# Kernel tuning notes

Measured on AMD Instinct MI355X. Metric: run time of the kernel, lower is better.

## Reference

```python
import jax, jax.numpy as jnp
import numpy as np

B, T, I, H, L = 32, 1024, 1024, 1024, 3


def setup_inputs() -> dict:
    key = jax.random.key(0)
    ks = jax.random.split(key, 8)
    sc_in = 1.0 / np.sqrt(I)
    sc_h = 1.0 / np.sqrt(H)
    return {
        "x": jax.random.normal(ks[0], (B, T, I), dtype=jnp.float32),
        "s0": jnp.zeros((B, H), dtype=jnp.float32),
        "w_h": jax.random.normal(ks[1], (I, H), dtype=jnp.float32) * sc_in,
        "w_t": jax.random.normal(ks[2], (I, H), dtype=jnp.float32) * sc_in,
        "w_c": jax.random.normal(ks[3], (I, H), dtype=jnp.float32) * sc_in,
        "Rh": jax.random.normal(ks[4], (L, H, H), dtype=jnp.float32) * sc_h,
        "Rt": jax.random.normal(ks[5], (L, H, H), dtype=jnp.float32) * sc_h,
        "Rc": jax.random.normal(ks[6], (L, H, H), dtype=jnp.float32) * sc_h,
        "bh": jnp.zeros((L, H), dtype=jnp.float32),
        "bt": jnp.zeros((L, H), dtype=jnp.float32),
        "bc": jnp.zeros((L, H), dtype=jnp.float32),
    }


def reference(x, s0, w_h, w_t, w_c, Rh, Rt, Rc, bh, bt, bc):
    # x: [B, T, I]; s0: [B, H]. Dropout prob = 0 -> identity.
    num_layers = Rh.shape[0]

    def step(s, x_t):
        # Input projections only feed layer 0 (as in the torch code).
        whx = x_t @ w_h  # [B, H]
        wtx = x_t @ w_t
        wcx = x_t @ w_c
        for l in range(num_layers):
            h_in = (whx if l == 0 else 0.0) + s @ Rh[l].T + bh[l]
            t_in = (wtx if l == 0 else 0.0) + s @ Rt[l].T + bt[l]
            c_in = (wcx if l == 0 else 0.0) + s @ Rc[l].T + bc[l]
            h = jnp.tanh(h_in)
            t = jax.nn.sigmoid(t_in)
            c = jax.nn.sigmoid(c_in)
            s = h * t + s * c
        return s, s

    x_tbi = jnp.swapaxes(x, 0, 1)  # [T, B, I] for scan over time
    s_T, outs = jax.lax.scan(step, s0, x_tbi)
    return jnp.swapaxes(outs, 0, 1), s_T  # ([B, T, H], [B, H])
```

## Files before the change

kernel.cpp:

```cpp
#include <hip/hip_runtime.h>
#include <hip/hip_bf16.h>

static constexpr int Bb = 32;
static constexpr int Tt = 1024;
static constexpr int Ii = 1024;
static constexpr int Hh = 1024;
static constexpr int NWG = 256;

static constexpr int SLOT_E = Hh * Bb;
static constexpr int NSLOT  = 3 * Tt + 1;

typedef float f4 __attribute__((ext_vector_type(4)));

static constexpr int LDS_WORDS = 36 * 1024 + 4 * 12 * 32;
static constexpr int LDS_BYTES = LDS_WORDS * 4;

template <typename PT> __device__ __forceinline__ float pt_to_f(PT v);
template <> __device__ __forceinline__ float pt_to_f<float>(float v) { return v; }
template <> __device__ __forceinline__ float pt_to_f<__hip_bfloat16>(__hip_bfloat16 v) { return __bfloat162float(v); }

template <typename PT> __device__ __forceinline__ PT f_to_pt(float v);
template <> __device__ __forceinline__ float f_to_pt<float>(float v) { return v; }
template <> __device__ __forceinline__ __hip_bfloat16 f_to_pt<__hip_bfloat16>(float v) { return __float2bfloat16(v); }

#define CGLD(dst, p, lit) \
    asm volatile("global_load_dwordx4 %0, %1, off offset:" lit : "=v"(dst) : "v"(p))
#define GB(sv, p, a,b,c,d2,e,f,g2,h) \
    CGLD(sv[0],p,a); CGLD(sv[1],p,b); CGLD(sv[2],p,c); CGLD(sv[3],p,d2); \
    CGLD(sv[4],p,e); CGLD(sv[5],p,f); CGLD(sv[6],p,g2); CGLD(sv[7],p,h)
#define VWAIT(n) do { asm volatile("s_waitcnt vmcnt(" #n ")" ::: "memory"); \
                      __builtin_amdgcn_sched_barrier(0); } while (0)

template <typename PT>
__global__ __launch_bounds__(256, 2) void proj_gemm(
    const float* __restrict__ X, const float* __restrict__ Wh,
    const float* __restrict__ Wt, const float* __restrict__ Wc,
    PT* __restrict__ P2)
{
    __shared__ float smem[4160];
    float* As = smem;
    float* Bs = smem + 1088;

    const int tid = threadIdx.x;
    const int tx = tid & 15, ty = tid >> 4;
    const int col0 = blockIdx.x * 64;
    const int t0 = blockIdx.y * 2;

    float acc[3][4][4];
#pragma unroll
    for (int g = 0; g < 3; ++g)
#pragma unroll
        for (int mm = 0; mm < 4; ++mm)
#pragma unroll
            for (int nn = 0; nn < 4; ++nn) acc[g][mm][nn] = 0.f;

    const int lm = tid >> 2, lk4 = (tid & 3) * 4;
    const float* aptr = X + ((size_t)(lm & 31) * Tt + (t0 + (lm >> 5))) * Ii + lk4;
    const int bk = tid >> 4, bn4 = (tid & 15) * 4;

    for (int k0 = 0; k0 < Ii; k0 += 16) {
        float4 av = *(const float4*)(aptr + k0);
        As[(lk4 + 0) * 68 + lm] = av.x;
        As[(lk4 + 1) * 68 + lm] = av.y;
        As[(lk4 + 2) * 68 + lm] = av.z;
        As[(lk4 + 3) * 68 + lm] = av.w;
        *(float4*)&Bs[0 * 1024 + bk * 64 + bn4] = *(const float4*)(Wh + (size_t)(k0 + bk) * Hh + col0 + bn4);
        *(float4*)&Bs[1 * 1024 + bk * 64 + bn4] = *(const float4*)(Wt + (size_t)(k0 + bk) * Hh + col0 + bn4);
        *(float4*)&Bs[2 * 1024 + bk * 64 + bn4] = *(const float4*)(Wc + (size_t)(k0 + bk) * Hh + col0 + bn4);
        __syncthreads();
#pragma unroll
        for (int k = 0; k < 16; ++k) {
            float4 a = *(const float4*)&As[k * 68 + ty * 4];
            float a_[4] = {a.x, a.y, a.z, a.w};
#pragma unroll
            for (int g = 0; g < 3; ++g) {
                float4 b = *(const float4*)&Bs[g * 1024 + k * 64 + tx * 4];
                float b_[4] = {b.x, b.y, b.z, b.w};
#pragma unroll
                for (int mm = 0; mm < 4; ++mm)
#pragma unroll
                    for (int nn = 0; nn < 4; ++nn)
                        acc[g][mm][nn] += a_[mm] * b_[nn];
            }
        }
        __syncthreads();
    }

    float* E = smem;
    const int b4 = (tid & 7) * 4;
#pragma unroll 1
    for (int g = 0; g < 3; ++g) {
        __syncthreads();
#pragma unroll
        for (int mm = 0; mm < 4; ++mm)
#pragma unroll
            for (int nn = 0; nn < 4; ++nn)
                E[(ty * 4 + mm) * 65 + tx * 4 + nn] = acc[g][mm][nn];
        __syncthreads();
        PT* dst = P2 + (size_t)g * Tt * Hh * Bb;
#pragma unroll
        for (int it = 0; it < 4; ++it) {
            const int line = (tid >> 3) + it * 32;
            const int tt = line >> 6, hh = line & 63;
            const float o0 = E[(tt * 32 + b4 + 0) * 65 + hh];
            const float o1 = E[(tt * 32 + b4 + 1) * 65 + hh];
            const float o2v = E[(tt * 32 + b4 + 2) * 65 + hh];
            const float o3 = E[(tt * 32 + b4 + 3) * 65 + hh];
            PT* d = dst + ((size_t)(t0 + tt) * Hh + col0 + hh) * Bb + b4;
            d[0] = f_to_pt<PT>(o0); d[1] = f_to_pt<PT>(o1);
            d[2] = f_to_pt<PT>(o2v); d[3] = f_to_pt<PT>(o3);
        }
    }
}

template <typename RT>
__global__ void init_k(const float* __restrict__ s0, RT* __restrict__ ring0,
                       unsigned* __restrict__ flags)
{
    const int i = blockIdx.x * 256 + threadIdx.x;
    if (i < Bb * Hh) { const int b = i >> 10, h = i & 1023; ring0[h * 32 + b] = f_to_pt<RT>(s0[i]); }
    if (i < 256) flags[i] = 0;
}

template <typename RT>
__global__ __launch_bounds__(256) void out_transpose(
    const RT* __restrict__ ring, float* __restrict__ out, float* __restrict__ sT)
{
    __shared__ float tile[128 * 33];
    const int tid = threadIdx.x;
    const int h0 = blockIdx.x * 128;
    const int t = blockIdx.y;
    const RT* src = ring + (size_t)(3 * t + 3) * SLOT_E + h0 * 32;
#pragma unroll
    for (int e = 0; e < 16; ++e) {
        const int idx = e * 256 + tid;
        tile[(idx >> 5) * 33 + (idx & 31)] = pt_to_f<RT>(src[idx]);
    }
    __syncthreads();
    const int hi = tid & 31, bq = tid >> 5;
#pragma unroll
    for (int e = 0; e < 4; ++e) {
        const int b = bq + e * 8;
        float4 v;
        v.x = tile[(hi * 4 + 0) * 33 + b];
        v.y = tile[(hi * 4 + 1) * 33 + b];
        v.z = tile[(hi * 4 + 2) * 33 + b];
        v.w = tile[(hi * 4 + 3) * 33 + b];
        *(float4*)(out + ((size_t)b * Tt + t) * Hh + h0 + hi * 4) = v;
        if (t == Tt - 1) *(float4*)(sT + (size_t)b * Hh + h0 + hi * 4) = v;
    }
}

template <typename PT, typename RT>
__global__ __launch_bounds__(256, 1) void rhn_recur(
    const float* __restrict__ Rh, const float* __restrict__ Rt,
    const float* __restrict__ Rc, const float* __restrict__ bh,
    const float* __restrict__ bt, const float* __restrict__ bc,
    const PT* __restrict__ P2, RT* __restrict__ ring,
    unsigned* __restrict__ flags)
{
    extern __shared__ float lds[];
    float* part = lds + 36 * 1024;

    const int g = blockIdx.x;
    const int tid = threadIdx.x;

    {
        const int k4 = tid * 4;
        const int sk = k4 ^ (((k4 >> 5) & 7) << 2);
#pragma unroll 1
        for (int j = 0; j < 36; ++j) {
            const int l = j / 12;
            const int rem = j - l * 12;
            const int gt = rem >> 2;
            const int q = rem & 3;
            const int h = (q << 8) | g;
            const float* src = (gt == 0 ? Rh : (gt == 1 ? Rt : Rc)) + ((size_t)l * Hh + h) * Hh;
            *(float4*)&lds[(j << 10) | sk] = *(const float4*)(src + k4);
        }
    }
    __syncthreads();

    const int ks = tid >> 3;
    const int b0 = (tid & 7) << 2;
    const int q8 = ks & 7;
    const int wv = tid >> 6;
    const int ub = tid & 31;
    const int uqc = (tid >> 5) & 3;
    const int uhc = (uqc << 8) | g;

    int o2[8];
#pragma unroll
    for (int c = 0; c < 8; ++c) o2[c] = ((c ^ q8) << 2);

    float brh[3], brt[3], brc[3];
#pragma unroll
    for (int l = 0; l < 3; ++l) {
        brh[l] = bh[l * Hh + uhc];
        brt[l] = bt[l * Hh + uhc];
        brc[l] = bc[l * Hh + uhc];
    }

    float so_reg = pt_to_f<RT>(ring[uhc * 32 + ub]);

#pragma unroll 1
    for (int t = 0; t < Tt; ++t) {
#pragma unroll 1
        for (int l = 0; l < 3; ++l) {
            const int p = t * 3 + l;

            float pv0 = 0.f, pv1 = 0.f, pv2 = 0.f;
            if (l == 0 && tid < 128) {
                const size_t pb = ((size_t)t * Hh + uhc) * Bb + ub;
                pv0 = pt_to_f<PT>(P2[pb]);
                pv1 = pt_to_f<PT>(P2[(size_t)Tt * Hh * Bb + pb]);
                pv2 = pt_to_f<PT>(P2[2 * (size_t)Tt * Hh * Bb + pb]);
            }

            const float* rp = lds + l * 12288 + (ks << 5);

            f4 accv[12];
#pragma unroll
            for (int jj = 0; jj < 12; ++jj) accv[jj] = (f4){0.f, 0.f, 0.f, 0.f};

            if constexpr (sizeof(RT) == 4) {
                const float* sA = (const float*)ring + (size_t)p * SLOT_E + (ks << 5) * 32 + b0;
                f4 sv0[8], sv1[8];
                GB(sv0, sA, "0","128","256","384","512","640","768","896");
                GB(sv1, sA, "1024","1152","1280","1408","1536","1664","1792","1920");
                VWAIT(8);
#pragma unroll
                for (int jj = 0; jj < 12; ++jj) {
                    const f4 r0 = *(const f4*)(rp + jj * 1024 + o2[0]);
                    const f4 r1 = *(const f4*)(rp + jj * 1024 + o2[1]);
                    f4 a = accv[jj];
                    a += sv0[0] * r0[0]; a += sv0[1] * r0[1]; a += sv0[2] * r0[2]; a += sv0[3] * r0[3];
                    a += sv0[4] * r1[0]; a += sv0[5] * r1[1]; a += sv0[6] * r1[2]; a += sv0[7] * r1[3];
                    accv[jj] = a;
                }
                GB(sv0, sA, "2048","2176","2304","2432","2560","2688","2816","2944");
                VWAIT(8);
#pragma unroll
                for (int jj = 0; jj < 12; ++jj) {
                    const f4 r0 = *(const f4*)(rp + jj * 1024 + o2[2]);
                    const f4 r1 = *(const f4*)(rp + jj * 1024 + o2[3]);
                    f4 a = accv[jj];
                    a += sv1[0] * r0[0]; a += sv1[1] * r0[1]; a += sv1[2] * r0[2]; a += sv1[3] * r0[3];
                    a += sv1[4] * r1[0]; a += sv1[5] * r1[1]; a += sv1[6] * r1[2]; a += sv1[7] * r1[3];
                    accv[jj] = a;
                }
                GB(sv1, sA, "3072","3200","3328","3456","3584","3712","3840","3968");
                VWAIT(8);
#pragma unroll
                for (int jj = 0; jj < 12; ++jj) {
                    const f4 r0 = *(const f4*)(rp + jj * 1024 + o2[4]);
                    const f4 r1 = *(const f4*)(rp + jj * 1024 + o2[5]);
                    f4 a = accv[jj];
                    a += sv0[0] * r0[0]; a += sv0[1] * r0[1]; a += sv0[2] * r0[2]; a += sv0[3] * r0[3];
                    a += sv0[4] * r1[0]; a += sv0[5] * r1[1]; a += sv0[6] * r1[2]; a += sv0[7] * r1[3];
                    accv[jj] = a;
                }
                VWAIT(0);
#pragma unroll
                for (int jj = 0; jj < 12; ++jj) {
                    const f4 r0 = *(const f4*)(rp + jj * 1024 + o2[6]);
                    const f4 r1 = *(const f4*)(rp + jj * 1024 + o2[7]);
                    f4 a = accv[jj];
                    a += sv1[0] * r0[0]; a += sv1[1] * r0[1]; a += sv1[2] * r0[2]; a += sv1[3] * r0[3];
                    a += sv1[4] * r1[0]; a += sv1[5] * r1[1]; a += sv1[6] * r1[2]; a += sv1[7] * r1[3];
                    accv[jj] = a;
                }
            } else {
                const __hip_bfloat16* sIn = (const __hip_bfloat16*)ring + (size_t)p * SLOT_E + (ks << 5) * 32 + b0;
#pragma unroll
                for (int blk = 0; blk < 4; ++blk) {
                    f4 sv[8];
#pragma unroll
                    for (int i = 0; i < 8; ++i) {
                        const ushort4 u = *(const ushort4*)(sIn + (blk * 8 + i) * 32);
                        sv[i][0] = __uint_as_float((unsigned)u.x << 16);
                        sv[i][1] = __uint_as_float((unsigned)u.y << 16);
                        sv[i][2] = __uint_as_float((unsigned)u.z << 16);
                        sv[i][3] = __uint_as_float((unsigned)u.w << 16);
                    }
#pragma unroll
                    for (int jj = 0; jj < 12; ++jj) {
                        const f4 r0 = *(const f4*)(rp + jj * 1024 + o2[blk * 2]);
                        const f4 r1 = *(const f4*)(rp + jj * 1024 + o2[blk * 2 + 1]);
                        f4 a = accv[jj];
                        a += sv[0] * r0[0]; a += sv[1] * r0[1]; a += sv[2] * r0[2]; a += sv[3] * r0[3];
                        a += sv[4] * r1[0]; a += sv[5] * r1[1]; a += sv[6] * r1[2]; a += sv[7] * r1[3];
                        accv[jj] = a;
                    }
                }
            }

#pragma unroll
            for (int jj = 0; jj < 12; ++jj) {
#pragma unroll
                for (int st = 8; st <= 32; st <<= 1) {
                    accv[jj][0] += __shfl_xor(accv[jj][0], st);
                    accv[jj][1] += __shfl_xor(accv[jj][1], st);
                    accv[jj][2] += __shfl_xor(accv[jj][2], st);
                    accv[jj][3] += __shfl_xor(accv[jj][3], st);
                }
            }
            f4 s1 = accv[0];
#pragma unroll
            for (int j2 = 1; j2 < 8; ++j2) if (q8 == j2) s1 = accv[j2];
            f4 s2 = accv[8];
#pragma unroll
            for (int j2 = 1; j2 < 4; ++j2) if (q8 == j2) s2 = accv[8 + j2];
            *(f4*)&part[(wv * 12 + q8) * 32 + b0] = s1;
            if (q8 < 4) *(f4*)&part[(wv * 12 + 8 + q8) * 32 + b0] = s2;
            __syncthreads();

            if (tid < 128) {
                float vals[3];
#pragma unroll
                for (int gt = 0; gt < 3; ++gt) {
                    const int jl = (gt << 2) + uqc;
                    vals[gt] = part[jl * 32 + ub] + part[(12 + jl) * 32 + ub]
                             + part[(24 + jl) * 32 + ub] + part[(36 + jl) * 32 + ub];
                }
                float bb0, bb1, bb2;
                if (l == 0)      { bb0 = brh[0]; bb1 = brt[0]; bb2 = brc[0]; }
                else if (l == 1) { bb0 = brh[1]; bb1 = brt[1]; bb2 = brc[1]; }
                else             { bb0 = brh[2]; bb1 = brt[2]; bb2 = brc[2]; }
                vals[0] += bb0; vals[1] += bb1; vals[2] += bb2;
                if (l == 0) { vals[0] += pv0; vals[1] += pv1; vals[2] += pv2; }
                const float hv = 1.f - 2.f / (1.f + __expf(2.f * vals[0]));
                const float tv = 1.f / (1.f + __expf(-vals[1]));
                const float cv = 1.f / (1.f + __expf(-vals[2]));
                const float sn = hv * tv + so_reg * cv;
                so_reg = sn;
                RT* wp = ring + (size_t)(p + 1) * SLOT_E + uhc * 32 + ub;
                if constexpr (sizeof(RT) == 4) {
                    __hip_atomic_store((float*)wp, sn, __ATOMIC_RELAXED, __HIP_MEMORY_SCOPE_AGENT);
                } else {
                    __hip_bfloat16 b16 = __float2bfloat16(sn);
                    __hip_atomic_store((unsigned short*)wp, *(unsigned short*)&b16,
                                       __ATOMIC_RELAXED, __HIP_MEMORY_SCOPE_AGENT);
                }
            }

            const unsigned ph = (unsigned)(p + 1);
            __syncthreads();
            if (tid == 0)
                __hip_atomic_store(&flags[g], ph, __ATOMIC_RELAXED, __HIP_MEMORY_SCOPE_AGENT);
            if (tid < 64) {
                for (;;) {
                    const unsigned v0 = __hip_atomic_load(&flags[tid],       __ATOMIC_RELAXED, __HIP_MEMORY_SCOPE_AGENT);
                    const unsigned v1 = __hip_atomic_load(&flags[tid + 64],  __ATOMIC_RELAXED, __HIP_MEMORY_SCOPE_AGENT);
                    const unsigned v2 = __hip_atomic_load(&flags[tid + 128], __ATOMIC_RELAXED, __HIP_MEMORY_SCOPE_AGENT);
                    const unsigned v3 = __hip_atomic_load(&flags[tid + 192], __ATOMIC_RELAXED, __HIP_MEMORY_SCOPE_AGENT);
                    if (__all((int)((v0 >= ph) & (v1 >= ph) & (v2 >= ph) & (v3 >= ph)))) break;
                    __builtin_amdgcn_s_sleep(2);
                }
            }
            __syncthreads();
        }
    }
}

extern "C" void kernel_launch(void* const* d_in, const int* in_sizes, int n_in,
                              void* d_out, int out_size, void* d_ws, size_t ws_size,
                              hipStream_t stream)
{
    (void)in_sizes; (void)n_in; (void)out_size;
    const float* x  = (const float*)d_in[0];
    const float* s0 = (const float*)d_in[1];
    const float* wh = (const float*)d_in[2];
    const float* wt = (const float*)d_in[3];
    const float* wc = (const float*)d_in[4];
    const float* Rh = (const float*)d_in[5];
    const float* Rt = (const float*)d_in[6];
    const float* Rc = (const float*)d_in[7];
    const float* bh = (const float*)d_in[8];
    const float* bt = (const float*)d_in[9];
    const float* bc = (const float*)d_in[10];

    float* out = (float*)d_out;
    float* sT  = out + (size_t)Bb * Tt * Hh;

    const size_t THB  = (size_t)Tt * Hh * Bb;
    const size_t p2f  = 3 * THB * 4, p2h = 3 * THB * 2;
    const size_t ringF = (size_t)NSLOT * SLOT_E * 4;
    const size_t ringH = (size_t)NSLOT * SLOT_E * 2;
    const size_t tail = 4096;

    char* w = (char*)d_ws;

    if (ws_size >= p2f + ringF + tail) {
        float* P2 = (float*)w;
        float* ring = (float*)(w + p2f);
        unsigned* flags = (unsigned*)(w + p2f + ringF);
        proj_gemm<float><<<dim3(16, 512), 256, 0, stream>>>(x, wh, wt, wc, P2);
        init_k<float><<<128, 256, 0, stream>>>(s0, ring, flags);
        hipFuncSetAttribute(reinterpret_cast<const void*>(rhn_recur<float, float>),
                            hipFuncAttributeMaxDynamicSharedMemorySize, LDS_BYTES);
        void* args[] = {(void*)&Rh, (void*)&Rt, (void*)&Rc, (void*)&bh, (void*)&bt, (void*)&bc,
                        (void*)&P2, (void*)&ring, (void*)&flags};
        hipLaunchCooperativeKernel(reinterpret_cast<void*>(rhn_recur<float, float>),
                                   dim3(NWG), dim3(256), args, LDS_BYTES, stream);
        out_transpose<float><<<dim3(8, 1024), 256, 0, stream>>>(ring, out, sT);
    } else if (ws_size >= p2h + ringF + tail) {
        __hip_bfloat16* P2 = (__hip_bfloat16*)w;
        float* ring = (float*)(w + p2h);
        unsigned* flags = (unsigned*)(w + p2h + ringF);
        proj_gemm<__hip_bfloat16><<<dim3(16, 512), 256, 0, stream>>>(x, wh, wt, wc, P2);
        init_k<float><<<128, 256, 0, stream>>>(s0, ring, flags);
        hipFuncSetAttribute(reinterpret_cast<const void*>(rhn_recur<__hip_bfloat16, float>),
                            hipFuncAttributeMaxDynamicSharedMemorySize, LDS_BYTES);
        void* args[] = {(void*)&Rh, (void*)&Rt, (void*)&Rc, (void*)&bh, (void*)&bt, (void*)&bc,
                        (void*)&P2, (void*)&ring, (void*)&flags};
        hipLaunchCooperativeKernel(reinterpret_cast<void*>(rhn_recur<__hip_bfloat16, float>),
                                   dim3(NWG), dim3(256), args, LDS_BYTES, stream);
        out_transpose<float><<<dim3(8, 1024), 256, 0, stream>>>(ring, out, sT);
    } else {
        __hip_bfloat16* P2 = (__hip_bfloat16*)w;
        __hip_bfloat16* ring = (__hip_bfloat16*)(w + p2h);
        unsigned* flags = (unsigned*)(w + p2h + ringH);
        proj_gemm<__hip_bfloat16><<<dim3(16, 512), 256, 0, stream>>>(x, wh, wt, wc, P2);
        init_k<__hip_bfloat16><<<128, 256, 0, stream>>>(s0, ring, flags);
        hipFuncSetAttribute(reinterpret_cast<const void*>(rhn_recur<__hip_bfloat16, __hip_bfloat16>),
                            hipFuncAttributeMaxDynamicSharedMemorySize, LDS_BYTES);
        void* args[] = {(void*)&Rh, (void*)&Rt, (void*)&Rc, (void*)&bh, (void*)&bt, (void*)&bc,
                        (void*)&P2, (void*)&ring, (void*)&flags};
        hipLaunchCooperativeKernel(reinterpret_cast<void*>(rhn_recur<__hip_bfloat16, __hip_bfloat16>),
                                   dim3(NWG), dim3(256), args, LDS_BYTES, stream);
        out_transpose<__hip_bfloat16><<<dim3(8, 1024), 256, 0, stream>>>(ring, out, sT);
    }
}
```

Measured before the change: 33.73 ms.

## Split batch into two independent halves with separate grid barriers to overlap sync

The recurrent kernel now splits the 32-sequence batch into two 16-sequence halves, each with its own state ring layout and its own set of per-workgroup flags. Each workgroup alternates between the halves, so the grid-wide barrier for one half can settle while the other half is computing. The aim is to hide the latency of the global flag barrier, which sits on the critical path of every one of the 3*T layer steps. In exchange there are twice as many barriers and smaller per-step work, and the flags are now cleared with a memset instead of inside the init kernel.

Result: no change. 33.34 ms (-1.2%).

```diff
diff --git a/kernel.cpp b/kernel.cpp
--- a/kernel.cpp
+++ b/kernel.cpp
@@ -7,13 +7,15 @@
 static constexpr int Hh = 1024;
 static constexpr int NWG = 256;
 
-static constexpr int SLOT_E = Hh * Bb;
-static constexpr int NSLOT  = 3 * Tt + 1;
+static constexpr int HSLOT = Hh * 16;
+static constexpr int NSLOT2 = 2 * (3 * Tt + 1);
 
 typedef float f4 __attribute__((ext_vector_type(4)));
 
-static constexpr int LDS_WORDS = 36 * 1024 + 4 * 12 * 32;
+static constexpr int LDS_WORDS = 36 * 1024 + 4 * 12 * 16;
 static constexpr int LDS_BYTES = LDS_WORDS * 4;
+
+static constexpr int SYNC_BYTES = 4096;
 
 template <typename PT> __device__ __forceinline__ float pt_to_f(PT v);
 template <> __device__ __forceinline__ float pt_to_f<float>(float v) { return v; }
@@ -25,9 +27,8 @@
 
 #define CGLD(dst, p, lit) \
     asm volatile("global_load_dwordx4 %0, %1, off offset:" lit : "=v"(dst) : "v"(p))
-#define GB(sv, p, a,b,c,d2,e,f,g2,h) \
-    CGLD(sv[0],p,a); CGLD(sv[1],p,b); CGLD(sv[2],p,c); CGLD(sv[3],p,d2); \
-    CGLD(sv[4],p,e); CGLD(sv[5],p,f); CGLD(sv[6],p,g2); CGLD(sv[7],p,h)
+#define GB4(sv, p, a,b,c,d2) \
+    CGLD(sv[0],p,a); CGLD(sv[1],p,b); CGLD(sv[2],p,c); CGLD(sv[3],p,d2)
 #define VWAIT(n) do { asm volatile("s_waitcnt vmcnt(" #n ")" ::: "memory"); \
                       __builtin_amdgcn_sched_barrier(0); } while (0)
 
@@ -114,12 +115,14 @@
 }
 
 template <typename RT>
-__global__ void init_k(const float* __restrict__ s0, RT* __restrict__ ring0,
-                       unsigned* __restrict__ flags)
+__global__ void init_k(const float* __restrict__ s0, RT* __restrict__ ring)
 {
     const int i = blockIdx.x * 256 + threadIdx.x;
-    if (i < Bb * Hh) { const int b = i >> 10, h = i & 1023; ring0[h * 32 + b] = f_to_pt<RT>(s0[i]); }
-    if (i < 256) flags[i] = 0;
+    if (i < Bb * Hh) {
+        const int b = i >> 10, h = i & 1023;
+        const int grp = b >> 4, bl = b & 15;
+        ring[(size_t)grp * HSLOT + h * 16 + bl] = f_to_pt<RT>(s0[i]);
+    }
 }
 
 template <typename RT>
@@ -130,11 +133,15 @@
     const int tid = threadIdx.x;
     const int h0 = blockIdx.x * 128;
     const int t = blockIdx.y;
-    const RT* src = ring + (size_t)(3 * t + 3) * SLOT_E + h0 * 32;
+    const RT* srcA = ring + (size_t)((3 * t + 3) * 2) * HSLOT + h0 * 16;
+    const RT* srcB = srcA + HSLOT;
 #pragma unroll
     for (int e = 0; e < 16; ++e) {
         const int idx = e * 256 + tid;
-        tile[(idx >> 5) * 33 + (idx & 31)] = pt_to_f<RT>(src[idx]);
+        const int h = idx >> 5, b = idx & 31;
+        const float v = (b < 16) ? pt_to_f<RT>(srcA[h * 16 + b])
+                                 : pt_to_f<RT>(srcB[h * 16 + (b - 16)]);
+        tile[h * 33 + b] = v;
     }
     __syncthreads();
     const int hi = tid & 31, bq = tid >> 5;
@@ -151,13 +158,28 @@
     }
 }
 
+__device__ __forceinline__ void poll256(unsigned* flags, int tid, unsigned ph)
+{
+    if (tid < 64) {
+        for (;;) {
+            const unsigned v0 = __hip_atomic_load(&flags[tid],       __ATOMIC_RELAXED, __HIP_MEMORY_SCOPE_AGENT);
+            const unsigned v1 = __hip_atomic_load(&flags[tid + 64],  __ATOMIC_RELAXED, __HIP_MEMORY_SCOPE_AGENT);
+            const unsigned v2 = __hip_atomic_load(&flags[tid + 128], __ATOMIC_RELAXED, __HIP_MEMORY_SCOPE_AGENT);
+            const unsigned v3 = __hip_atomic_load(&flags[tid + 192], __ATOMIC_RELAXED, __HIP_MEMORY_SCOPE_AGENT);
+            if (__all((int)((v0 >= ph) & (v1 >= ph) & (v2 >= ph) & (v3 >= ph)))) break;
+            __builtin_amdgcn_s_sleep(2);
+        }
+    }
+    __syncthreads();
+}
+
 template <typename PT, typename RT>
 __global__ __launch_bounds__(256, 1) void rhn_recur(
     const float* __restrict__ Rh, const float* __restrict__ Rt,
     const float* __restrict__ Rc, const float* __restrict__ bh,
     const float* __restrict__ bt, const float* __restrict__ bc,
     const PT* __restrict__ P2, RT* __restrict__ ring,
-    unsigned* __restrict__ flags)
+    unsigned* __restrict__ flagsA, unsigned* __restrict__ flagsB)
 {
     extern __shared__ float lds[];
     float* part = lds + 36 * 1024;
@@ -167,7 +189,7 @@
 
     {
         const int k4 = tid * 4;
-        const int sk = k4 ^ (((k4 >> 5) & 7) << 2);
+        const int sk = k4 ^ (((k4 >> 5) & 3) << 2);
 #pragma unroll 1
         for (int j = 0; j < 36; ++j) {
             const int l = j / 12;
@@ -181,17 +203,19 @@
     }
     __syncthreads();
 
-    const int ks = tid >> 3;
-    const int b0 = (tid & 7) << 2;
-    const int q8 = ks & 7;
+    const int ks = tid >> 2;
+    const int bq = tid & 3;
+    const int b0 = bq << 2;
     const int wv = tid >> 6;
-    const int ub = tid & 31;
-    const int uqc = (tid >> 5) & 3;
-    const int uhc = (uqc << 8) | g;
-
-    int o2[8];
-#pragma unroll
-    for (int c = 0; c < 8; ++c) o2[c] = ((c ^ q8) << 2);
+    const int jsel = ks & 15;
+    const int ubb = tid & 15;
+    const int uq  = (tid >> 4) & 3;
+    const int uhc = (uq << 8) | g;
+
+    int o2[4];
+#pragma unroll
+    for (int c = 0; c < 4; ++c)
+        o2[c] = (((ks << 4) | (c << 2))) ^ ((((ks << 4) >> 5) & 3) << 2);
 
     float brh[3], brt[3], brc[3];
 #pragma unroll
@@ -201,164 +225,162 @@
         brc[l] = bc[l * Hh + uhc];
     }
 
-    float so_reg = pt_to_f<RT>(ring[uhc * 32 + ub]);
+    float soA = pt_to_f<RT>(ring[uhc * 16 + ubb]);
+    float soB = pt_to_f<RT>(ring[(size_t)HSLOT + uhc * 16 + ubb]);
+
+    const size_t THB = (size_t)Tt * Hh * Bb;
+    float pvA0 = 0.f, pvA1 = 0.f, pvA2 = 0.f, pvB0 = 0.f, pvB1 = 0.f, pvB2 = 0.f;
+    auto loadP = [&](int tt) {
+        if (tid < 64) {
+            const size_t pb = ((size_t)tt * Hh + uhc) * Bb + ubb;
+            pvA0 = pt_to_f<PT>(P2[pb]);
+            pvA1 = pt_to_f<PT>(P2[THB + pb]);
+            pvA2 = pt_to_f<PT>(P2[2 * THB + pb]);
+            pvB0 = pt_to_f<PT>(P2[pb + 16]);
+            pvB1 = pt_to_f<PT>(P2[THB + pb + 16]);
+            pvB2 = pt_to_f<PT>(P2[2 * THB + pb + 16]);
+        }
+    };
+    loadP(0);
+
+    auto halfstep = [&](const float* rp, const RT* rs, RT* rw, float& so,
+                        float pv0, float pv1, float pv2, bool addP,
+                        float bb0, float bb1, float bb2) {
+        f4 accv[12];
+#pragma unroll
+        for (int jj = 0; jj < 12; ++jj) accv[jj] = (f4){0.f, 0.f, 0.f, 0.f};
+
+        if constexpr (sizeof(RT) == 4) {
+            const float* sA = (const float*)rs + (size_t)(ks << 4) * 16 + b0;
+            f4 sv0[4], sv1[4], sv2[4], sv3[4];
+            GB4(sv0, sA, "0","64","128","192");
+            GB4(sv1, sA, "256","320","384","448");
+            GB4(sv2, sA, "512","576","640","704");
+            GB4(sv3, sA, "768","832","896","960");
+            VWAIT(12);
+#pragma unroll
+            for (int jj = 0; jj < 12; ++jj) {
+                const f4 r = *(const f4*)(rp + jj * 1024 + o2[0]);
+                f4 a = accv[jj];
+                a += sv0[0] * r[0]; a += sv0[1] * r[1]; a += sv0[2] * r[2]; a += sv0[3] * r[3];
+                accv[jj] = a;
+            }
+            VWAIT(8);
+#pragma unroll
+            for (int jj = 0; jj < 12; ++jj) {
+                const f4 r = *(const f4*)(rp + jj * 1024 + o2[1]);
+                f4 a = accv[jj];
+                a += sv1[0] * r[0]; a += sv1[1] * r[1]; a += sv1[2] * r[2]; a += sv1[3] * r[3];
+                accv[jj] = a;
+            }
+            VWAIT(4);
+#pragma unroll
+            for (int jj = 0; jj < 12; ++jj) {
+                const f4 r = *(const f4*)(rp + jj * 1024 + o2[2]);
+                f4 a = accv[jj];
+                a += sv2[0] * r[0]; a += sv2[1] * r[1]; a += sv2[2] * r[2]; a += sv2[3] * r[3];
+                accv[jj] = a;
+            }
+            VWAIT(0);
+#pragma unroll
+            for (int jj = 0; jj < 12; ++jj) {
+                const f4 r = *(const f4*)(rp + jj * 1024 + o2[3]);
+                f4 a = accv[jj];
+                a += sv3[0] * r[0]; a += sv3[1] * r[1]; a += sv3[2] * r[2]; a += sv3[3] * r[3];
+                accv[jj] = a;
+            }
+        } else {
+            const __hip_bfloat16* sIn = (const __hip_bfloat16*)rs + (size_t)(ks << 4) * 16 + b0;
+#pragma unroll
+            for (int blk = 0; blk < 4; ++blk) {
+                f4 sv[4];
+#pragma unroll
+                for (int i = 0; i < 4; ++i) {
+                    const ushort4 u = *(const ushort4*)(sIn + (size_t)(blk * 4 + i) * 16);
+                    sv[i][0] = __uint_as_float((unsigned)u.x << 16);
+                    sv[i][1] = __uint_as_float((unsigned)u.y << 16);
+                    sv[i][2] = __uint_as_float((unsigned)u.z << 16);
+                    sv[i][3] = __uint_as_float((unsigned)u.w << 16);
+                }
+#pragma unroll
+                for (int jj = 0; jj < 12; ++jj) {
+                    const f4 r = *(const f4*)(rp + jj * 1024 + o2[blk]);
+                    f4 a = accv[jj];
+                    a += sv[0] * r[0]; a += sv[1] * r[1]; a += sv[2] * r[2]; a += sv[3] * r[3];
+                    accv[jj] = a;
+                }
+            }
+        }
+
+#pragma unroll
+        for (int jj = 0; jj < 12; ++jj) {
+#pragma unroll
+            for (int st = 4; st <= 32; st <<= 1) {
+                accv[jj][0] += __shfl_xor(accv[jj][0], st);
+                accv[jj][1] += __shfl_xor(accv[jj][1], st);
+                accv[jj][2] += __shfl_xor(accv[jj][2], st);
+                accv[jj][3] += __shfl_xor(accv[jj][3], st);
+            }
+        }
+        f4 s1 = accv[0];
+#pragma unroll
+        for (int j2 = 1; j2 < 12; ++j2) if (jsel == j2) s1 = accv[j2];
+        if (jsel < 12) *(f4*)&part[wv * 192 + jsel * 16 + b0] = s1;
+        __syncthreads();
+
+        if (tid < 64) {
+            float vals[3];
+#pragma unroll
+            for (int gt = 0; gt < 3; ++gt) {
+                const int jl = (gt << 2) + uq;
+                vals[gt] = part[jl * 16 + ubb] + part[192 + jl * 16 + ubb]
+                         + part[384 + jl * 16 + ubb] + part[576 + jl * 16 + ubb];
+            }
+            vals[0] += bb0; vals[1] += bb1; vals[2] += bb2;
+            if (addP) { vals[0] += pv0; vals[1] += pv1; vals[2] += pv2; }
+            const float hv = 1.f - 2.f / (1.f + __expf(2.f * vals[0]));
+            const float tv = 1.f / (1.f + __expf(-vals[1]));
+            const float cv = 1.f / (1.f + __expf(-vals[2]));
+            const float sn = hv * tv + so * cv;
+            so = sn;
+            RT* wp = rw + uhc * 16 + ubb;
+            if constexpr (sizeof(RT) == 4) {
+                __hip_atomic_store((float*)wp, sn, __ATOMIC_RELAXED, __HIP_MEMORY_SCOPE_AGENT);
+            } else {
+                __hip_bfloat16 b16 = __float2bfloat16(sn);
+                __hip_atomic_store((unsigned short*)wp, *(unsigned short*)&b16,
+                                   __ATOMIC_RELAXED, __HIP_MEMORY_SCOPE_AGENT);
+            }
+        }
+        __syncthreads();
+    };
 
 #pragma unroll 1
     for (int t = 0; t < Tt; ++t) {
 #pragma unroll 1
         for (int l = 0; l < 3; ++l) {
             const int p = t * 3 + l;
-
-            float pv0 = 0.f, pv1 = 0.f, pv2 = 0.f;
-            if (l == 0 && tid < 128) {
-                const size_t pb = ((size_t)t * Hh + uhc) * Bb + ub;
-                pv0 = pt_to_f<PT>(P2[pb]);
-                pv1 = pt_to_f<PT>(P2[(size_t)Tt * Hh * Bb + pb]);
-                pv2 = pt_to_f<PT>(P2[2 * (size_t)Tt * Hh * Bb + pb]);
-            }
-
-            const float* rp = lds + l * 12288 + (ks << 5);
-
-            f4 accv[12];
-#pragma unroll
-            for (int jj = 0; jj < 12; ++jj) accv[jj] = (f4){0.f, 0.f, 0.f, 0.f};
-
-            if constexpr (sizeof(RT) == 4) {
-                const float* sA = (const float*)ring + (size_t)p * SLOT_E + (ks << 5) * 32 + b0;
-                f4 sv0[8], sv1[8];
-                GB(sv0, sA, "0","128","256","384","512","640","768","896");
-                GB(sv1, sA, "1024","1152","1280","1408","1536","1664","1792","1920");
-                VWAIT(8);
-#pragma unroll
-                for (int jj = 0; jj < 12; ++jj) {
-                    const f4 r0 = *(const f4*)(rp + jj * 1024 + o2[0]);
-                    const f4 r1 = *(const f4*)(rp + jj * 1024 + o2[1]);
-                    f4 a = accv[jj];
-                    a += sv0[0] * r0[0]; a += sv0[1] * r0[1]; a += sv0[2] * r0[2]; a += sv0[3] * r0[3];
-                    a += sv0[4] * r1[0]; a += sv0[5] * r1[1]; a += sv0[6] * r1[2]; a += sv0[7] * r1[3];
-                    accv[jj] = a;
-                }
-                GB(sv0, sA, "2048","2176","2304","2432","2560","2688","2816","2944");
-                VWAIT(8);
-#pragma unroll
-                for (int jj = 0; jj < 12; ++jj) {
-                    const f4 r0 = *(const f4*)(rp + jj * 1024 + o2[2]);
-                    const f4 r1 = *(const f4*)(rp + jj * 1024 + o2[3]);
-                    f4 a = accv[jj];
-                    a += sv1[0] * r0[0]; a += sv1[1] * r0[1]; a += sv1[2] * r0[2]; a += sv1[3] * r0[3];
-                    a += sv1[4] * r1[0]; a += sv1[5] * r1[1]; a += sv1[6] * r1[2]; a += sv1[7] * r1[3];
-                    accv[jj] = a;
-                }
-                GB(sv1, sA, "3072","3200","3328","3456","3584","3712","3840","3968");
-                VWAIT(8);
-#pragma unroll
-                for (int jj = 0; jj < 12; ++jj) {
-                    const f4 r0 = *(const f4*)(rp + jj * 1024 + o2[4]);
-                    const f4 r1 = *(const f4*)(rp + jj * 1024 + o2[5]);
-                    f4 a = accv[jj];
-                    a += sv0[0] * r0[0]; a += sv0[1] * r0[1]; a += sv0[2] * r0[2]; a += sv0[3] * r0[3];
-                    a += sv0[4] * r1[0]; a += sv0[5] * r1[1]; a += sv0[6] * r1[2]; a += sv0[7] * r1[3];
-                    accv[jj] = a;
-                }
-                VWAIT(0);
-#pragma unroll
-                for (int jj = 0; jj < 12; ++jj) {
-                    const f4 r0 = *(const f4*)(rp + jj * 1024 + o2[6]);
-                    const f4 r1 = *(const f4*)(rp + jj * 1024 + o2[7]);
-                    f4 a = accv[jj];
-                    a += sv1[0] * r0[0]; a += sv1[1] * r0[1]; a += sv1[2] * r0[2]; a += sv1[3] * r0[3];
-                    a += sv1[4] * r1[0]; a += sv1[5] * r1[1]; a += sv1[6] * r1[2]; a += sv1[7] * r1[3];
-                    accv[jj] = a;
-                }
-            } else {
-                const __hip_bfloat16* sIn = (const __hip_bfloat16*)ring + (size_t)p * SLOT_E + (ks << 5) * 32 + b0;
-#pragma unroll
-                for (int blk = 0; blk < 4; ++blk) {
-                    f4 sv[8];
-#pragma unroll
-                    for (int i = 0; i < 8; ++i) {
-                        const ushort4 u = *(const ushort4*)(sIn + (blk * 8 + i) * 32);
-                        sv[i][0] = __uint_as_float((unsigned)u.x << 16);
-                        sv[i][1] = __uint_as_float((unsigned)u.y << 16);
-                        sv[i][2] = __uint_as_float((unsigned)u.z << 16);
-                        sv[i][3] = __uint_as_float((unsigned)u.w << 16);
-                    }
-#pragma unroll
-                    for (int jj = 0; jj < 12; ++jj) {
-                        const f4 r0 = *(const f4*)(rp + jj * 1024 + o2[blk * 2]);
-                        const f4 r1 = *(const f4*)(rp + jj * 1024 + o2[blk * 2 + 1]);
-                        f4 a = accv[jj];
-                        a += sv[0] * r0[0]; a += sv[1] * r0[1]; a += sv[2] * r0[2]; a += sv[3] * r0[3];
-                        a += sv[4] * r1[0]; a += sv[5] * r1[1]; a += sv[6] * r1[2]; a += sv[7] * r1[3];
-                        accv[jj] = a;
-                    }
-                }
-            }
-
-#pragma unroll
-            for (int jj = 0; jj < 12; ++jj) {
-#pragma unroll
-                for (int st = 8; st <= 32; st <<= 1) {
-                    accv[jj][0] += __shfl_xor(accv[jj][0], st);
-                    accv[jj][1] += __shfl_xor(accv[jj][1], st);
-                    accv[jj][2] += __shfl_xor(accv[jj][2], st);
-                    accv[jj][3] += __shfl_xor(accv[jj][3], st);
-                }
-            }
-            f4 s1 = accv[0];
-#pragma unroll
-            for (int j2 = 1; j2 < 8; ++j2) if (q8 == j2) s1 = accv[j2];
-            f4 s2 = accv[8];
-#pragma unroll
-            for (int j2 = 1; j2 < 4; ++j2) if (q8 == j2) s2 = accv[8 + j2];
-            *(f4*)&part[(wv * 12 + q8) * 32 + b0] = s1;
-            if (q8 < 4) *(f4*)&part[(wv * 12 + 8 + q8) * 32 + b0] = s2;
-            __syncthreads();
-
-            if (tid < 128) {
-                float vals[3];
-#pragma unroll
-                for (int gt = 0; gt < 3; ++gt) {
-                    const int jl = (gt << 2) + uqc;
-                    vals[gt] = part[jl * 32 + ub] + part[(12 + jl) * 32 + ub]
-                             + part[(24 + jl) * 32 + ub] + part[(36 + jl) * 32 + ub];
-                }
-                float bb0, bb1, bb2;
-                if (l == 0)      { bb0 = brh[0]; bb1 = brt[0]; bb2 = brc[0]; }
-                else if (l == 1) { bb0 = brh[1]; bb1 = brt[1]; bb2 = brc[1]; }
-                else             { bb0 = brh[2]; bb1 = brt[2]; bb2 = brc[2]; }
-                vals[0] += bb0; vals[1] += bb1; vals[2] += bb2;
-                if (l == 0) { vals[0] += pv0; vals[1] += pv1; vals[2] += pv2; }
-                const float hv = 1.f - 2.f / (1.f + __expf(2.f * vals[0]));
-                const float tv = 1.f / (1.f + __expf(-vals[1]));
-                const float cv = 1.f / (1.f + __expf(-vals[2]));
-                const float sn = hv * tv + so_reg * cv;
-                so_reg = sn;
-                RT* wp = ring + (size_t)(p + 1) * SLOT_E + uhc * 32 + ub;
-                if constexpr (sizeof(RT) == 4) {
-                    __hip_atomic_store((float*)wp, sn, __ATOMIC_RELAXED, __HIP_MEMORY_SCOPE_AGENT);
-                } else {
-                    __hip_bfloat16 b16 = __float2bfloat16(sn);
-                    __hip_atomic_store((unsigned short*)wp, *(unsigned short*)&b16,
-                                       __ATOMIC_RELAXED, __HIP_MEMORY_SCOPE_AGENT);
-                }
-            }
-
-            const unsigned ph = (unsigned)(p + 1);
-            __syncthreads();
+            float bb0, bb1, bb2;
+            if (l == 0)      { bb0 = brh[0]; bb1 = brt[0]; bb2 = brc[0]; }
+            else if (l == 1) { bb0 = brh[1]; bb1 = brt[1]; bb2 = brc[1]; }
+            else             { bb0 = brh[2]; bb1 = brt[2]; bb2 = brc[2]; }
+            const float* rp = lds + l * 12288;
+
+            poll256(flagsA, tid, (unsigned)p);
+            halfstep(rp, ring + (size_t)(p * 2 + 0) * HSLOT,
+                         ring + (size_t)((p + 1) * 2 + 0) * HSLOT,
+                     soA, pvA0, pvA1, pvA2, l == 0, bb0, bb1, bb2);
             if (tid == 0)
-                __hip_atomic_store(&flags[g], ph, __ATOMIC_RELAXED, __HIP_MEMORY_SCOPE_AGENT);
-            if (tid < 64) {
-                for (;;) {
-                    const unsigned v0 = __hip_atomic_load(&flags[tid],       __ATOMIC_RELAXED, __HIP_MEMORY_SCOPE_AGENT);
-                    const unsigned v1 = __hip_atomic_load(&flags[tid + 64],  __ATOMIC_RELAXED, __HIP_MEMORY_SCOPE_AGENT);
-                    const unsigned v2 = __hip_atomic_load(&flags[tid + 128], __ATOMIC_RELAXED, __HIP_MEMORY_SCOPE_AGENT);
-                    const unsigned v3 = __hip_atomic_load(&flags[tid + 192], __ATOMIC_RELAXED, __HIP_MEMORY_SCOPE_AGENT);
-                    if (__all((int)((v0 >= ph) & (v1 >= ph) & (v2 >= ph) & (v3 >= ph)))) break;
-                    __builtin_amdgcn_s_sleep(2);
-                }
-            }
-            __syncthreads();
+                __hip_atomic_store(&flagsA[g], (unsigned)(p + 1), __ATOMIC_RELAXED, __HIP_MEMORY_SCOPE_AGENT);
+
+            poll256(flagsB, tid, (unsigned)p);
+            halfstep(rp, ring + (size_t)(p * 2 + 1) * HSLOT,
+                         ring + (size_t)((p + 1) * 2 + 1) * HSLOT,
+                     soB, pvB0, pvB1, pvB2, l == 0, bb0, bb1, bb2);
+            if (tid == 0)
+                __hip_atomic_store(&flagsB[g], (unsigned)(p + 1), __ATOMIC_RELAXED, __HIP_MEMORY_SCOPE_AGENT);
+
+            if (l == 2 && t + 1 < Tt) loadP(t + 1);
         }
     }
 }
@@ -385,48 +407,53 @@
 
     const size_t THB  = (size_t)Tt * Hh * Bb;
     const size_t p2f  = 3 * THB * 4, p2h = 3 * THB * 2;
-    const size_t ringF = (size_t)NSLOT * SLOT_E * 4;
-    const size_t ringH = (size_t)NSLOT * SLOT_E * 2;
-    const size_t tail = 4096;
+    const size_t ringF = (size_t)NSLOT2 * HSLOT * 4;
+    const size_t ringH = (size_t)NSLOT2 * HSLOT * 2;
 
     char* w = (char*)d_ws;
 
-    if (ws_size >= p2f + ringF + tail) {
+    if (ws_size >= p2f + ringF + SYNC_BYTES) {
         float* P2 = (float*)w;
         float* ring = (float*)(w + p2f);
-        unsigned* flags = (unsigned*)(w + p2f + ringF);
+        unsigned* flagsA = (unsigned*)(w + p2f + ringF);
+        unsigned* flagsB = flagsA + 256;
+        hipMemsetAsync(flagsA, 0, SYNC_BYTES, stream);
         proj_gemm<float><<<dim3(16, 512), 256, 0, stream>>>(x, wh, wt, wc, P2);
-        init_k<float><<<128, 256, 0, stream>>>(s0, ring, flags);
+        init_k<float><<<128, 256, 0, stream>>>(s0, ring);
         hipFuncSetAttribute(reinterpret_cast<const void*>(rhn_recur<float, float>),
                             hipFuncAttributeMaxDynamicSharedMemorySize, LDS_BYTES);
         void* args[] = {(void*)&Rh, (void*)&Rt, (void*)&Rc, (void*)&bh, (void*)&bt, (void*)&bc,
-                        (void*)&P2, (void*)&ring, (void*)&flags};
+                        (void*)&P2, (void*)&ring, (void*)&flagsA, (void*)&flagsB};
         hipLaunchCooperativeKernel(reinterpret_cast<void*>(rhn_recur<float, float>),
                                    dim3(NWG), dim3(256), args, LDS_BYTES, stream);
         out_transpose<float><<<dim3(8, 1024), 256, 0, stream>>>(ring, out, sT);
-    } else if (ws_size >= p2h + ringF + tail) {
+    } else if (ws_size >= p2h + ringF + SYNC_BYTES) {
         __hip_bfloat16* P2 = (__hip_bfloat16*)w;
         float* ring = (float*)(w + p2h);
-        unsigned* flags = (unsigned*)(w + p2h + ringF);
+        unsigned* flagsA = (unsigned*)(w + p2h + ringF);
+        unsigned* flagsB = flagsA + 256;
+        hipMemsetAsync(flagsA, 0, SYNC_BYTES, stream);
         proj_gemm<__hip_bfloat16><<<dim3(16, 512), 256, 0, stream>>>(x, wh, wt, wc, P2);
-        init_k<float><<<128, 256, 0, stream>>>(s0, ring, flags);
+        init_k<float><<<128, 256, 0, stream>>>(s0, ring);
         hipFuncSetAttribute(reinterpret_cast<const void*>(rhn_recur<__hip_bfloat16, float>),
                             hipFuncAttributeMaxDynamicSharedMemorySize, LDS_BYTES);
         void* args[] = {(void*)&Rh, (void*)&Rt, (void*)&Rc, (void*)&bh, (void*)&bt, (void*)&bc,
-                        (void*)&P2, (void*)&ring, (void*)&flags};
+                        (void*)&P2, (void*)&ring, (void*)&flagsA, (void*)&flagsB};
         hipLaunchCooperativeKernel(reinterpret_cast<void*>(rhn_recur<__hip_bfloat16, float>),
                                    dim3(NWG), dim3(256), args, LDS_BYTES, stream);
         out_transpose<float><<<dim3(8, 1024), 256, 0, stream>>>(ring, out, sT);
     } else {
         __hip_bfloat16* P2 = (__hip_bfloat16*)w;
         __hip_bfloat16* ring = (__hip_bfloat16*)(w + p2h);
-        unsigned* flags = (unsigned*)(w + p2h + ringH);
+        unsigned* flagsA = (unsigned*)(w + p2h + ringH);
+        unsigned* flagsB = flagsA + 256;
+        hipMemsetAsync(flagsA, 0, SYNC_BYTES, stream);
         proj_gemm<__hip_bfloat16><<<dim3(16, 512), 256, 0, stream>>>(x, wh, wt, wc, P2);
-        init_k<__hip_bfloat16><<<128, 256, 0, stream>>>(s0, ring, flags);
+        init_k<__hip_bfloat16><<<128, 256, 0, stream>>>(s0, ring);
         hipFuncSetAttribute(reinterpret_cast<const void*>(rhn_recur<__hip_bfloat16, __hip_bfloat16>),
                             hipFuncAttributeMaxDynamicSharedMemorySize, LDS_BYTES);
         void* args[] = {(void*)&Rh, (void*)&Rt, (void*)&Rc, (void*)&bh, (void*)&bt, (void*)&bc,
-                        (void*)&P2, (void*)&ring, (void*)&flags};
+                        (void*)&P2, (void*)&ring, (void*)&flagsA, (void*)&flagsB};
         hipLaunchCooperativeKernel(reinterpret_cast<void*>(rhn_recur<__hip_bfloat16, __hip_bfloat16>),
                                    dim3(NWG), dim3(256), args, LDS_BYTES, stream);
         out_transpose<__hip_bfloat16><<<dim3(8, 1024), 256, 0, stream>>>(ring, out, sT);
```

## Replace grid-wide flag barrier with sentinel-polled dataflow sync on ring slots

Applied to the files above, without the earlier changes.

Drops the per-layer-step global flag barrier. Each ring slot is now pre-filled with a NaN sentinel, and consumers poll their loaded state chunks with system-coherent loads until no sentinel remains. The LDS partial buffer is double-buffered by step parity so the next step can start without a block-wide barrier. This removes barrier latency from the critical path. In exchange it adds a large sentinel-fill pass over the whole ring, the chance of spinning on a partially written slot, and reliance on the sentinel never appearing as a real value.

After: 32.00 ms. -5.1%, faster.

```diff
diff --git a/kernel.cpp b/kernel.cpp
--- a/kernel.cpp
+++ b/kernel.cpp
@@ -12,8 +12,11 @@
 
 typedef float f4 __attribute__((ext_vector_type(4)));
 
-static constexpr int LDS_WORDS = 36 * 1024 + 4 * 12 * 32;
+static constexpr int LDS_WORDS = 36 * 1024 + 2 * 1536;
 static constexpr int LDS_BYTES = LDS_WORDS * 4;
+
+static constexpr unsigned SENT32 = 0x7FC0DEADu;
+static constexpr unsigned SENT16 = 0x7FC1u;
 
 template <typename PT> __device__ __forceinline__ float pt_to_f(PT v);
 template <> __device__ __forceinline__ float pt_to_f<float>(float v) { return v; }
@@ -23,13 +26,37 @@
 template <> __device__ __forceinline__ float f_to_pt<float>(float v) { return v; }
 template <> __device__ __forceinline__ __hip_bfloat16 f_to_pt<__hip_bfloat16>(float v) { return __float2bfloat16(v); }
 
-#define CGLD(dst, p, lit) \
-    asm volatile("global_load_dwordx4 %0, %1, off offset:" lit : "=v"(dst) : "v"(p))
-#define GB(sv, p, a,b,c,d2,e,f,g2,h) \
-    CGLD(sv[0],p,a); CGLD(sv[1],p,b); CGLD(sv[2],p,c); CGLD(sv[3],p,d2); \
-    CGLD(sv[4],p,e); CGLD(sv[5],p,f); CGLD(sv[6],p,g2); CGLD(sv[7],p,h)
+#define BGLD(dst, p, lit) \
+    asm volatile("global_load_dwordx4 %0, %1, off offset:" lit " sc0 sc1" : "=v"(dst) : "v"(p))
+#define BG8(sv, p, a,b,c,d2,e,f,g2,h) \
+    BGLD(sv[0],p,a); BGLD(sv[1],p,b); BGLD(sv[2],p,c); BGLD(sv[3],p,d2); \
+    BGLD(sv[4],p,e); BGLD(sv[5],p,f); BGLD(sv[6],p,g2); BGLD(sv[7],p,h)
+#define BGLD2(dst, p, lit) \
+    asm volatile("global_load_dwordx2 %0, %1, off offset:" lit " sc0 sc1" : "=v"(dst) : "v"(p))
+#define BG8x2(su, p, a,b,c,d2,e,f,g2,h) \
+    BGLD2(su[0],p,a); BGLD2(su[1],p,b); BGLD2(su[2],p,c); BGLD2(su[3],p,d2); \
+    BGLD2(su[4],p,e); BGLD2(su[5],p,f); BGLD2(su[6],p,g2); BGLD2(su[7],p,h)
 #define VWAIT(n) do { asm volatile("s_waitcnt vmcnt(" #n ")" ::: "memory"); \
                       __builtin_amdgcn_sched_barrier(0); } while (0)
+
+__device__ __forceinline__ int grp_ok32(const f4* sv) {
+    int ok = 1;
+#pragma unroll
+    for (int i = 0; i < 8; ++i)
+#pragma unroll
+        for (int j = 0; j < 4; ++j)
+            ok &= (__float_as_uint(sv[i][j]) != SENT32);
+    return ok;
+}
+__device__ __forceinline__ int grp_ok16(const uint2* su) {
+    int ok = 1;
+#pragma unroll
+    for (int i = 0; i < 8; ++i) {
+        ok &= ((su[i].x & 0xFFFFu) != SENT16) & ((su[i].x >> 16) != SENT16);
+        ok &= ((su[i].y & 0xFFFFu) != SENT16) & ((su[i].y >> 16) != SENT16);
+    }
+    return ok;
+}
 
 template <typename PT>
 __global__ __launch_bounds__(256, 2) void proj_gemm(
@@ -114,12 +141,20 @@
 }
 
 template <typename RT>
-__global__ void init_k(const float* __restrict__ s0, RT* __restrict__ ring0,
-                       unsigned* __restrict__ flags)
+__global__ __launch_bounds__(256) void init_ring(const float* __restrict__ s0,
+                                                 RT* __restrict__ ring)
 {
-    const int i = blockIdx.x * 256 + threadIdx.x;
-    if (i < Bb * Hh) { const int b = i >> 10, h = i & 1023; ring0[h * 32 + b] = f_to_pt<RT>(s0[i]); }
-    if (i < 256) flags[i] = 0;
+    const size_t tid = (size_t)blockIdx.x * 256 + threadIdx.x;
+    if (tid < (size_t)Bb * Hh) {
+        const int b = (int)(tid >> 10), h = (int)(tid & 1023);
+        ring[h * 32 + b] = f_to_pt<RT>(s0[tid]);
+    }
+    const unsigned sw = (sizeof(RT) == 4) ? SENT32 : ((SENT16 << 16) | SENT16);
+    const uint4 pat = {sw, sw, sw, sw};
+    uint4* base = (uint4*)(ring + SLOT_E);
+    const size_t n16 = (size_t)(NSLOT - 1) * SLOT_E * sizeof(RT) / 16;
+    const size_t stride = (size_t)gridDim.x * 256;
+    for (size_t i = tid; i < n16; i += stride) base[i] = pat;
 }
 
 template <typename RT>
@@ -156,11 +191,9 @@
     const float* __restrict__ Rh, const float* __restrict__ Rt,
     const float* __restrict__ Rc, const float* __restrict__ bh,
     const float* __restrict__ bt, const float* __restrict__ bc,
-    const PT* __restrict__ P2, RT* __restrict__ ring,
-    unsigned* __restrict__ flags)
+    const PT* __restrict__ P2, RT* __restrict__ ring)
 {
     extern __shared__ float lds[];
-    float* part = lds + 36 * 1024;
 
     const int g = blockIdx.x;
     const int tid = threadIdx.x;
@@ -208,6 +241,7 @@
 #pragma unroll 1
         for (int l = 0; l < 3; ++l) {
             const int p = t * 3 + l;
+            float* part = lds + 36 * 1024 + (p & 1) * 1536;
 
             float pv0 = 0.f, pv1 = 0.f, pv2 = 0.f;
             if (l == 0 && tid < 128) {
@@ -226,9 +260,14 @@
             if constexpr (sizeof(RT) == 4) {
                 const float* sA = (const float*)ring + (size_t)p * SLOT_E + (ks << 5) * 32 + b0;
                 f4 sv0[8], sv1[8];
-                GB(sv0, sA, "0","128","256","384","512","640","768","896");
-                GB(sv1, sA, "1024","1152","1280","1408","1536","1664","1792","1920");
+                BG8(sv0, sA, "0","128","256","384","512","640","768","896");
+                BG8(sv1, sA, "1024","1152","1280","1408","1536","1664","1792","1920");
                 VWAIT(8);
+                while (!__all(grp_ok32(sv0))) {
+                    __builtin_amdgcn_s_sleep(1);
+                    BG8(sv0, sA, "0","128","256","384","512","640","768","896");
+                    VWAIT(0);
+                }
 #pragma unroll
                 for (int jj = 0; jj < 12; ++jj) {
                     const f4 r0 = *(const f4*)(rp + jj * 1024 + o2[0]);
@@ -238,8 +277,13 @@
                     a += sv0[4] * r1[0]; a += sv0[5] * r1[1]; a += sv0[6] * r1[2]; a += sv0[7] * r1[3];
                     accv[jj] = a;
                 }
-                GB(sv0, sA, "2048","2176","2304","2432","2560","2688","2816","2944");
+                BG8(sv0, sA, "2048","2176","2304","2432","2560","2688","2816","2944");
                 VWAIT(8);
+                while (!__all(grp_ok32(sv1))) {
+                    __builtin_amdgcn_s_sleep(1);
+                    BG8(sv1, sA, "1024","1152","1280","1408","1536","1664","1792","1920");
+                    VWAIT(0);
+                }
 #pragma unroll
                 for (int jj = 0; jj < 12; ++jj) {
                     const f4 r0 = *(const f4*)(rp + jj * 1024 + o2[2]);
@@ -249,8 +293,13 @@
                     a += sv1[4] * r1[0]; a += sv1[5] * r1[1]; a += sv1[6] * r1[2]; a += sv1[7] * r1[3];
                     accv[jj] = a;
                 }
-                GB(sv1, sA, "3072","3200","3328","3456","3584","3712","3840","3968");
+                BG8(sv1, sA, "3072","3200","3328","3456","3584","3712","3840","3968");
                 VWAIT(8);
+                while (!__all(grp_ok32(sv0))) {
+                    __builtin_amdgcn_s_sleep(1);
+                    BG8(sv0, sA, "2048","2176","2304","2432","2560","2688","2816","2944");
+                    VWAIT(0);
+                }
 #pragma unroll
                 for (int jj = 0; jj < 12; ++jj) {
                     const f4 r0 = *(const f4*)(rp + jj * 1024 + o2[4]);
@@ -261,6 +310,11 @@
                     accv[jj] = a;
                 }
                 VWAIT(0);
+                while (!__all(grp_ok32(sv1))) {
+                    __builtin_amdgcn_s_sleep(1);
+                    BG8(sv1, sA, "3072","3200","3328","3456","3584","3712","3840","3968");
+                    VWAIT(0);
+                }
 #pragma unroll
                 for (int jj = 0; jj < 12; ++jj) {
                     const f4 r0 = *(const f4*)(rp + jj * 1024 + o2[6]);
@@ -272,16 +326,24 @@
                 }
             } else {
                 const __hip_bfloat16* sIn = (const __hip_bfloat16*)ring + (size_t)p * SLOT_E + (ks << 5) * 32 + b0;
-#pragma unroll
+#pragma unroll 1
                 for (int blk = 0; blk < 4; ++blk) {
+                    uint2 su[8];
+                    const __hip_bfloat16* pb2 = sIn + (size_t)blk * 256;
+                    BG8x2(su, pb2, "0","64","128","192","256","320","384","448");
+                    VWAIT(0);
+                    while (!__all(grp_ok16(su))) {
+                        __builtin_amdgcn_s_sleep(1);
+                        BG8x2(su, pb2, "0","64","128","192","256","320","384","448");
+                        VWAIT(0);
+                    }
                     f4 sv[8];
 #pragma unroll
                     for (int i = 0; i < 8; ++i) {
-                        const ushort4 u = *(const ushort4*)(sIn + (blk * 8 + i) * 32);
-                        sv[i][0] = __uint_as_float((unsigned)u.x << 16);
-                        sv[i][1] = __uint_as_float((unsigned)u.y << 16);
-                        sv[i][2] = __uint_as_float((unsigned)u.z << 16);
-                        sv[i][3] = __uint_as_float((unsigned)u.w << 16);
+                        sv[i][0] = __uint_as_float(su[i].x << 16);
+                        sv[i][1] = __uint_as_float(su[i].x & 0xFFFF0000u);
+                        sv[i][2] = __uint_as_float(su[i].y << 16);
+                        sv[i][3] = __uint_as_float(su[i].y & 0xFFFF0000u);
                     }
 #pragma unroll
                     for (int jj = 0; jj < 12; ++jj) {
@@ -343,22 +405,6 @@
                                        __ATOMIC_RELAXED, __HIP_MEMORY_SCOPE_AGENT);
                 }
             }
-
-            const unsigned ph = (unsigned)(p + 1);
-            __syncthreads();
-            if (tid == 0)
-                __hip_atomic_store(&flags[g], ph, __ATOMIC_RELAXED, __HIP_MEMORY_SCOPE_AGENT);
-            if (tid < 64) {
-                for (;;) {
-                    const unsigned v0 = __hip_atomic_load(&flags[tid],       __ATOMIC_RELAXED, __HIP_MEMORY_SCOPE_AGENT);
-                    const unsigned v1 = __hip_atomic_load(&flags[tid + 64],  __ATOMIC_RELAXED, __HIP_MEMORY_SCOPE_AGENT);
-                    const unsigned v2 = __hip_atomic_load(&flags[tid + 128], __ATOMIC_RELAXED, __HIP_MEMORY_SCOPE_AGENT);
-                    const unsigned v3 = __hip_atomic_load(&flags[tid + 192], __ATOMIC_RELAXED, __HIP_MEMORY_SCOPE_AGENT);
-                    if (__all((int)((v0 >= ph) & (v1 >= ph) & (v2 >= ph) & (v3 >= ph)))) break;
-                    __builtin_amdgcn_s_sleep(2);
-                }
-            }
-            __syncthreads();
         }
     }
 }
@@ -387,46 +433,42 @@
     const size_t p2f  = 3 * THB * 4, p2h = 3 * THB * 2;
     const size_t ringF = (size_t)NSLOT * SLOT_E * 4;
     const size_t ringH = (size_t)NSLOT * SLOT_E * 2;
-    const size_t tail = 4096;
 
     char* w = (char*)d_ws;
 
-    if (ws_size >= p2f + ringF + tail) {
+    if (ws_size >= p2f + ringF) {
         float* P2 = (float*)w;
         float* ring = (float*)(w + p2f);
-        unsigned* flags = (unsigned*)(w + p2f + ringF);
         proj_gemm<float><<<dim3(16, 512), 256, 0, stream>>>(x, wh, wt, wc, P2);
-        init_k<float><<<128, 256, 0, stream>>>(s0, ring, flags);
+        init_ring<float><<<2048, 256, 0, stream>>>(s0, ring);
         hipFuncSetAttribute(reinterpret_cast<const void*>(rhn_recur<float, float>),
                             hipFuncAttributeMaxDynamicSharedMemorySize, LDS_BYTES);
         void* args[] = {(void*)&Rh, (void*)&Rt, (void*)&Rc, (void*)&bh, (void*)&bt, (void*)&bc,
-                        (void*)&P2, (void*)&ring, (void*)&flags};
+                        (void*)&P2, (void*)&ring};
         hipLaunchCooperativeKernel(reinterpret_cast<void*>(rhn_recur<float, float>),
                                    dim3(NWG), dim3(256), args, LDS_BYTES, stream);
         out_transpose<float><<<dim3(8, 1024), 256, 0, stream>>>(ring, out, sT);
-    } else if (ws_size >= p2h + ringF + tail) {
+    } else if (ws_size >= p2h + ringF) {
         __hip_bfloat16* P2 = (__hip_bfloat16*)w;
         float* ring = (float*)(w + p2h);
-        unsigned* flags = (unsigned*)(w + p2h + ringF);
         proj_gemm<__hip_bfloat16><<<dim3(16, 512), 256, 0, stream>>>(x, wh, wt, wc, P2);
-        init_k<float><<<128, 256, 0, stream>>>(s0, ring, flags);
+        init_ring<float><<<2048, 256, 0, stream>>>(s0, ring);
         hipFuncSetAttribute(reinterpret_cast<const void*>(rhn_recur<__hip_bfloat16, float>),
                             hipFuncAttributeMaxDynamicSharedMemorySize, LDS_BYTES);
         void* args[] = {(void*)&Rh, (void*)&Rt, (void*)&Rc, (void*)&bh, (void*)&bt, (void*)&bc,
-                        (void*)&P2, (void*)&ring, (void*)&flags};
+                        (void*)&P2, (void*)&ring};
         hipLaunchCooperativeKernel(reinterpret_cast<void*>(rhn_recur<__hip_bfloat16, float>),
                                    dim3(NWG), dim3(256), args, LDS_BYTES, stream);
         out_transpose<float><<<dim3(8, 1024), 256, 0, stream>>>(ring, out, sT);
     } else {
         __hip_bfloat16* P2 = (__hip_bfloat16*)w;
         __hip_bfloat16* ring = (__hip_bfloat16*)(w + p2h);
-        unsigned* flags = (unsigned*)(w + p2h + ringH);
         proj_gemm<__hip_bfloat16><<<dim3(16, 512), 256, 0, stream>>>(x, wh, wt, wc, P2);
-        init_k<__hip_bfloat16><<<128, 256, 0, stream>>>(s0, ring, flags);
+        init_ring<__hip_bfloat16><<<2048, 256, 0, stream>>>(s0, ring);
         hipFuncSetAttribute(reinterpret_cast<const void*>(rhn_recur<__hip_bfloat16, __hip_bfloat16>),
                             hipFuncAttributeMaxDynamicSharedMemorySize, LDS_BYTES);
         void* args[] = {(void*)&Rh, (void*)&Rt, (void*)&Rc, (void*)&bh, (void*)&bt, (void*)&bc,
-                        (void*)&P2, (void*)&ring, (void*)&flags};
+                        (void*)&P2, (void*)&ring};
         hipLaunchCooperativeKernel(reinterpret_cast<void*>(rhn_recur<__hip_bfloat16, __hip_bfloat16>),
                                    dim3(NWG), dim3(256), args, LDS_BYTES, stream);
         out_transpose<__hip_bfloat16><<<dim3(8, 1024), 256, 0, stream>>>(ring, out, sT);
```
